# Kernel optimization log

Hardware: AMD Instinct MI355X
Metric: run time of the kernel (lower is better)

## Reference

```python
import jax, jax.numpy as jnp
import numpy as np

B, IN, H = 64, 1024, 1024

def setup_inputs() -> dict:
    key = jax.random.key(0)
    ks = jax.random.split(key, 16)
    s = 0.02
    inp = {
        'x': jax.random.normal(ks[0], (B, IN), dtype=jnp.float32),
        'C': jax.random.normal(ks[1], (B, H, H), dtype=jnp.float32) * 0.1,
        'n': jax.random.normal(ks[2], (B, H), dtype=jnp.float32) * 0.1,
        'm': jnp.zeros((B, H), dtype=jnp.float32),
    }
    names = ['i', 'f', 'o', 'q', 'k', 'v']
    for j, nm in enumerate(names):
        inp['W_' + nm] = jax.random.normal(ks[3 + 2 * j], (H, IN), dtype=jnp.float32) * s
        inp['b_' + nm] = jax.random.normal(ks[4 + 2 * j], (H,), dtype=jnp.float32) * s
    return inp

def reference(x, C, n, m, W_i, b_i, W_f, b_f, W_o, b_o, W_q, b_q, W_k, b_k, W_v, b_v):
    lin = lambda W, b: x @ W.T + b  # (B, H)
    i_tilda = lin(W_i, b_i)
    f_tilda = lin(W_f, b_f)
    o_tilda = lin(W_o, b_o)
    q_t = lin(W_q, b_q)
    k_t = lin(W_k, b_k) / jnp.sqrt(jnp.asarray(H, dtype=x.dtype))
    v_t = lin(W_v, b_v)

    f_t = jax.nn.sigmoid(f_tilda)
    o_t = jax.nn.sigmoid(o_tilda)
    # m_t = max(log(f_t) + m, log(exp(i_tilda))) = max(log_sigmoid(f_tilda) + m, i_tilda)
    m_t = jnp.maximum(jnp.log(f_t) + m, i_tilda)
    i_prime = jnp.exp(i_tilda - m_t)

    # Outer-product fast-weight update: C_t[b,i,k] = f*C + i' * v[b,i] k[b,k]
    C_t = f_t[:, :, None] * C + i_prime[:, :, None] * jnp.einsum('bi,bk->bik', v_t, k_t)
    n_t = f_t * n + i_prime * k_t

    # diagonal(n_t @ q_t.T) == per-row dot product
    normalize_inner = jnp.sum(n_t * q_t, axis=-1)
    divisor = jnp.maximum(jnp.abs(normalize_inner), jnp.ones_like(normalize_inner))
    h_tilda = jnp.einsum('bkj,bj->bk', C_t, q_t) / divisor[:, None]
    h_t = o_t * h_tilda
    return (h_t, C_t, n_t, m_t)
```

## Files before the change

### kernel.cpp

```cpp
#include <hip/hip_runtime.h>
#include <math.h>

#define BB 64
#define HH 1024
#define KK 1024

#define OFF_H ((size_t)0)
#define OFF_C ((size_t)BB * HH)
#define OFF_N (OFF_C + (size_t)BB * HH * HH)
#define OFF_M (OFF_N + (size_t)BB * HH)

#define SPLITK 4
#define GBN 32
#define GBK 64
#define NCOLBLK (6 * HH / GBN)

__device__ __forceinline__ float dot4(float4 a, float4 b) {
    return a.x * b.x + a.y * b.y + a.z * b.z + a.w * b.w;
}
__device__ __forceinline__ void fma4(float4& a, const float4 x, const float4 w) {
    a.x = fmaf(x.x, w.x, a.x);
    a.y = fmaf(x.y, w.y, a.y);
    a.z = fmaf(x.z, w.z, a.z);
    a.w = fmaf(x.w, w.w, a.w);
}

__global__ __launch_bounds__(256) void k_gemm(
    const float* __restrict__ x,
    const float* __restrict__ Wi, const float* __restrict__ Wf,
    const float* __restrict__ Wo, const float* __restrict__ Wq,
    const float* __restrict__ Wk, const float* __restrict__ Wv,
    float* __restrict__ Gp)
{
    const int cb = blockIdx.x % NCOLBLK;
    const int kc = blockIdx.x / NCOLBLK;
    const int n0 = cb * GBN;
    const int g  = n0 >> 10;
    const int h0 = n0 & (HH - 1);
    const int k0 = kc * (KK / SPLITK);

    const float* W = (g == 0) ? Wi : (g == 1) ? Wf : (g == 2) ? Wo
                   : (g == 3) ? Wq : (g == 4) ? Wk : Wv;

    const int tid = threadIdx.x;
    const int tn  = tid & 15;
    const int tm  = tid >> 4;

    __shared__ float sW[GBN][GBK + 4];

    float4 acc[4][2];
#pragma unroll
    for (int i = 0; i < 4; ++i)
#pragma unroll
        for (int j = 0; j < 2; ++j) acc[i][j] = make_float4(0.f, 0.f, 0.f, 0.f);

    for (int kk = k0; kk < k0 + KK / SPLITK; kk += GBK) {
#pragma unroll
        for (int i = 0; i < 2; ++i) {
            const int idx = tid + i * 256;
            const int c = idx >> 4;
            const int s = idx & 15;
            const float4 v = *(const float4*)(W + (size_t)(h0 + c) * KK + kk + s * 4);
            *(float4*)&sW[c][s * 4] = v;
        }
        __syncthreads();

        const float4* xr0 = (const float4*)(x + (size_t)(tm * 4 + 0) * KK + kk);
        const float4* xr1 = (const float4*)(x + (size_t)(tm * 4 + 1) * KK + kk);
        const float4* xr2 = (const float4*)(x + (size_t)(tm * 4 + 2) * KK + kk);
        const float4* xr3 = (const float4*)(x + (size_t)(tm * 4 + 3) * KK + kk);
#pragma unroll
        for (int s = 0; s < GBK / 4; ++s) {
            const float4 w0 = *(const float4*)&sW[tn * 2 + 0][s * 4];
            const float4 w1 = *(const float4*)&sW[tn * 2 + 1][s * 4];
            const float4 a0 = xr0[s];
            const float4 a1 = xr1[s];
            const float4 a2 = xr2[s];
            const float4 a3 = xr3[s];
            fma4(acc[0][0], a0, w0); fma4(acc[0][1], a0, w1);
            fma4(acc[1][0], a1, w0); fma4(acc[1][1], a1, w1);
            fma4(acc[2][0], a2, w0); fma4(acc[2][1], a2, w1);
            fma4(acc[3][0], a3, w0); fma4(acc[3][1], a3, w1);
        }
        __syncthreads();
    }

#pragma unroll
    for (int i = 0; i < 4; ++i) {
        const int b = tm * 4 + i;
        const int h = h0 + tn * 2;
        float2 v;
        v.x = acc[i][0].x + acc[i][0].y + acc[i][0].z + acc[i][0].w;
        v.y = acc[i][1].x + acc[i][1].y + acc[i][1].z + acc[i][1].w;
        *(float2*)(Gp + ((size_t)(kc * 6 + g) * BB + b) * HH + h) = v;
    }
}

__global__ __launch_bounds__(256) void k_epilogue(
    const float* __restrict__ Gp,
    const float* __restrict__ n_in, const float* __restrict__ m_in,
    const float* __restrict__ bi, const float* __restrict__ bf,
    const float* __restrict__ bo, const float* __restrict__ bq,
    const float* __restrict__ bk, const float* __restrict__ bv,
    float* __restrict__ out,
    float* __restrict__ f_s, float* __restrict__ iv_s, float* __restrict__ o_s,
    float* __restrict__ k_s, float* __restrict__ q_s, float* __restrict__ ni)
{
    const int b = blockIdx.x >> 2;
    const int h = ((blockIdx.x & 3) << 8) + threadIdx.x;
    const size_t bh = (size_t)b * HH + h;

    float gsum[6];
#pragma unroll
    for (int gg = 0; gg < 6; ++gg) {
        float s = 0.f;
#pragma unroll
        for (int kc = 0; kc < SPLITK; ++kc)
            s += Gp[((size_t)(kc * 6 + gg) * BB + b) * HH + h];
        gsum[gg] = s;
    }

    const float it = gsum[0] + bi[h];
    const float ft = gsum[1] + bf[h];
    const float ot = gsum[2] + bo[h];
    const float qt = gsum[3] + bq[h];
    const float kt = (gsum[4] + bk[h]) * 0.03125f;
    const float vt = gsum[5] + bv[h];

    const float fsig = 1.0f / (1.0f + expf(-ft));
    const float lsf  = (ft >= 0.0f) ? -log1pf(expf(-ft)) : (ft - log1pf(expf(ft)));
    const float mt   = fmaxf(lsf + m_in[bh], it);
    const float ip   = expf(it - mt);
    const float nt   = fsig * n_in[bh] + ip * kt;
    const float osg  = 1.0f / (1.0f + expf(-ot));

    out[OFF_N + bh] = nt;
    out[OFF_M + bh] = mt;
    f_s[bh]  = fsig;
    iv_s[bh] = ip * vt;
    o_s[bh]  = osg;
    k_s[bh]  = kt;
    q_s[bh]  = qt;

    float d = nt * qt;
#pragma unroll
    for (int off = 32; off >= 1; off >>= 1) d += __shfl_xor(d, off, 64);
    __shared__ float sd[4];
    if ((threadIdx.x & 63) == 0) sd[threadIdx.x >> 6] = d;
    __syncthreads();
    if (threadIdx.x == 0) atomicAdd(ni + b, sd[0] + sd[1] + sd[2] + sd[3]);
}

__global__ __launch_bounds__(256) void k2_fastweight(
    const float* __restrict__ C,
    const float* __restrict__ f_s, const float* __restrict__ iv_s,
    const float* __restrict__ o_s, const float* __restrict__ k_s,
    const float* __restrict__ q_s, const float* __restrict__ ni,
    float* __restrict__ out)
{
    const int b    = blockIdx.y;
    const int wave = threadIdx.x >> 6;
    const int lane = threadIdx.x & 63;
    const int i0   = blockIdx.x * 64 + wave * 16;

    const float4* kr = (const float4*)(k_s + (size_t)b * HH);
    const float4* qr = (const float4*)(q_s + (size_t)b * HH);
    float4 kv[4], qv[4];
#pragma unroll
    for (int s = 0; s < 4; ++s) {
        kv[s] = kr[lane + s * 64];
        qv[s] = qr[lane + s * 64];
    }
    const float inv_div = 1.0f / fmaxf(fabsf(ni[b]), 1.0f);

#pragma unroll 2
    for (int r = 0; r < 16; ++r) {
        const int row = b * HH + i0 + r;
        const float f  = f_s[row];
        const float iv = iv_s[row];
        const float4* Cr = (const float4*)(C + (size_t)row * HH);
        float4*       Ct = (float4*)(out + OFF_C + (size_t)row * HH);
        float d = 0.f;
#pragma unroll
        for (int s = 0; s < 4; ++s) {
            const float4 c4 = Cr[lane + s * 64];
            float4 o;
            o.x = fmaf(f, c4.x, iv * kv[s].x);
            o.y = fmaf(f, c4.y, iv * kv[s].y);
            o.z = fmaf(f, c4.z, iv * kv[s].z);
            o.w = fmaf(f, c4.w, iv * kv[s].w);
            Ct[lane + s * 64] = o;
            d += dot4(o, qv[s]);
        }
#pragma unroll
        for (int off = 32; off >= 1; off >>= 1) d += __shfl_xor(d, off, 64);
        if (lane == 0) out[OFF_H + row] = o_s[row] * d * inv_div;
    }
}

extern "C" void kernel_launch(void* const* d_in, const int* in_sizes, int n_in,
                              void* d_out, int out_size, void* d_ws, size_t ws_size,
                              hipStream_t stream) {
    const float* x  = (const float*)d_in[0];
    const float* C  = (const float*)d_in[1];
    const float* n  = (const float*)d_in[2];
    const float* m  = (const float*)d_in[3];
    const float* Wi = (const float*)d_in[4];  const float* bi = (const float*)d_in[5];
    const float* Wf = (const float*)d_in[6];  const float* bf = (const float*)d_in[7];
    const float* Wo = (const float*)d_in[8];  const float* bo = (const float*)d_in[9];
    const float* Wq = (const float*)d_in[10]; const float* bq = (const float*)d_in[11];
    const float* Wk = (const float*)d_in[12]; const float* bk = (const float*)d_in[13];
    const float* Wv = (const float*)d_in[14]; const float* bv = (const float*)d_in[15];

    float* out = (float*)d_out;
    float* ws  = (float*)d_ws;
    float* f_s  = ws;
    float* iv_s = ws + (size_t)BB * HH;
    float* o_s  = ws + (size_t)2 * BB * HH;
    float* k_s  = ws + (size_t)3 * BB * HH;
    float* q_s  = ws + (size_t)4 * BB * HH;
    float* ni   = ws + (size_t)5 * BB * HH;
    float* Gp   = ws + (size_t)5 * BB * HH + 256;

    hipMemsetAsync(ni, 0, BB * sizeof(float), stream);

    k_gemm<<<NCOLBLK * SPLITK, 256, 0, stream>>>(x, Wi, Wf, Wo, Wq, Wk, Wv, Gp);

    k_epilogue<<<BB * 4, 256, 0, stream>>>(Gp, n, m, bi, bf, bo, bq, bk, bv,
                                           out, f_s, iv_s, o_s, k_s, q_s, ni);

    k2_fastweight<<<dim3(16, BB), 256, 0, stream>>>(C, f_s, iv_s, o_s, k_s, q_s, ni, out);
}
```

Measured before the change: 520.2 us.

## Use nontemporal C streaming, prefetch rows, double fastweight grid, drop atomic memset

New measurement: 494.2 us. 1.05x faster.

```diff
diff --git a/kernel.cpp b/kernel.cpp
--- a/kernel.cpp
+++ b/kernel.cpp
@@ -15,6 +15,11 @@
 #define GBK 64
 #define NCOLBLK (6 * HH / GBN)
 
+typedef float __attribute__((ext_vector_type(4))) f32x4;
+
+__device__ __forceinline__ float dot4v(f32x4 a, f32x4 b) {
+    return a[0] * b[0] + a[1] * b[1] + a[2] * b[2] + a[3] * b[3];
+}
 __device__ __forceinline__ float dot4(float4 a, float4 b) {
     return a.x * b.x + a.y * b.y + a.z * b.z + a.w * b.w;
 }
@@ -23,6 +28,12 @@
     a.y = fmaf(x.y, w.y, a.y);
     a.z = fmaf(x.z, w.z, a.z);
     a.w = fmaf(x.w, w.w, a.w);
+}
+__device__ __forceinline__ f32x4 ntload4(const float* p) {
+    return __builtin_nontemporal_load((const f32x4*)p);
+}
+__device__ __forceinline__ void ntstore4(float* p, f32x4 v) {
+    __builtin_nontemporal_store(v, (f32x4*)p);
 }
 
 __global__ __launch_bounds__(256) void k_gemm(
@@ -60,8 +71,8 @@
             const int idx = tid + i * 256;
             const int c = idx >> 4;
             const int s = idx & 15;
-            const float4 v = *(const float4*)(W + (size_t)(h0 + c) * KK + kk + s * 4);
-            *(float4*)&sW[c][s * 4] = v;
+            const f32x4 v = ntload4(W + (size_t)(h0 + c) * KK + kk + s * 4);
+            *(f32x4*)&sW[c][s * 4] = v;
         }
         __syncthreads();
 
@@ -104,7 +115,7 @@
     const float* __restrict__ bk, const float* __restrict__ bv,
     float* __restrict__ out,
     float* __restrict__ f_s, float* __restrict__ iv_s, float* __restrict__ o_s,
-    float* __restrict__ k_s, float* __restrict__ q_s, float* __restrict__ ni)
+    float* __restrict__ k_s, float* __restrict__ q_s, float* __restrict__ ni4)
 {
     const int b = blockIdx.x >> 2;
     const int h = ((blockIdx.x & 3) << 8) + threadIdx.x;
@@ -148,53 +159,75 @@
     __shared__ float sd[4];
     if ((threadIdx.x & 63) == 0) sd[threadIdx.x >> 6] = d;
     __syncthreads();
-    if (threadIdx.x == 0) atomicAdd(ni + b, sd[0] + sd[1] + sd[2] + sd[3]);
+    if (threadIdx.x == 0)
+        ni4[blockIdx.x] = sd[0] + sd[1] + sd[2] + sd[3];
 }
 
 __global__ __launch_bounds__(256) void k2_fastweight(
     const float* __restrict__ C,
     const float* __restrict__ f_s, const float* __restrict__ iv_s,
     const float* __restrict__ o_s, const float* __restrict__ k_s,
-    const float* __restrict__ q_s, const float* __restrict__ ni,
+    const float* __restrict__ q_s, const float* __restrict__ ni4,
     float* __restrict__ out)
 {
     const int b    = blockIdx.y;
     const int wave = threadIdx.x >> 6;
     const int lane = threadIdx.x & 63;
-    const int i0   = blockIdx.x * 64 + wave * 16;
-
-    const float4* kr = (const float4*)(k_s + (size_t)b * HH);
-    const float4* qr = (const float4*)(q_s + (size_t)b * HH);
-    float4 kv[4], qv[4];
+    const int i0   = blockIdx.x * 32 + wave * 8;
+
+    const float* kr = k_s + (size_t)b * HH;
+    const float* qr = q_s + (size_t)b * HH;
+    f32x4 kv[4], qv[4];
 #pragma unroll
     for (int s = 0; s < 4; ++s) {
-        kv[s] = kr[lane + s * 64];
-        qv[s] = qr[lane + s * 64];
-    }
-    const float inv_div = 1.0f / fmaxf(fabsf(ni[b]), 1.0f);
-
-#pragma unroll 2
-    for (int r = 0; r < 16; ++r) {
-        const int row = b * HH + i0 + r;
-        const float f  = f_s[row];
-        const float iv = iv_s[row];
-        const float4* Cr = (const float4*)(C + (size_t)row * HH);
-        float4*       Ct = (float4*)(out + OFF_C + (size_t)row * HH);
+        kv[s] = *(const f32x4*)(kr + lane * 4 + s * 256);
+        qv[s] = *(const f32x4*)(qr + lane * 4 + s * 256);
+    }
+    const float inv_div = 1.0f /
+        fmaxf(fabsf(ni4[b * 4] + ni4[b * 4 + 1] + ni4[b * 4 + 2] + ni4[b * 4 + 3]), 1.0f);
+
+    const size_t base = (size_t)b * HH + i0;
+    float fr[8], ivr[8], ogr[8];
+#pragma unroll
+    for (int r = 0; r < 8; ++r) {
+        fr[r]  = f_s[base + r];
+        ivr[r] = iv_s[base + r];
+        ogr[r] = o_s[base + r] * inv_div;
+    }
+
+    const float* Crow = C + base * HH;
+    float* Ctrow = out + OFF_C + base * HH;
+
+    f32x4 c_cur[4], c_nxt[4];
+#pragma unroll
+    for (int s = 0; s < 4; ++s) c_cur[s] = ntload4(Crow + lane * 4 + s * 256);
+
+#pragma unroll
+    for (int r = 0; r < 8; ++r) {
+        if (r < 7) {
+            const float* Cn = Crow + (size_t)(r + 1) * HH;
+#pragma unroll
+            for (int s = 0; s < 4; ++s) c_nxt[s] = ntload4(Cn + lane * 4 + s * 256);
+        }
+        const float f  = fr[r];
+        const float iv = ivr[r];
+        float* Ct = Ctrow + (size_t)r * HH;
         float d = 0.f;
 #pragma unroll
         for (int s = 0; s < 4; ++s) {
-            const float4 c4 = Cr[lane + s * 64];
-            float4 o;
-            o.x = fmaf(f, c4.x, iv * kv[s].x);
-            o.y = fmaf(f, c4.y, iv * kv[s].y);
-            o.z = fmaf(f, c4.z, iv * kv[s].z);
-            o.w = fmaf(f, c4.w, iv * kv[s].w);
-            Ct[lane + s * 64] = o;
-            d += dot4(o, qv[s]);
+            f32x4 o;
+            o[0] = fmaf(f, c_cur[s][0], iv * kv[s][0]);
+            o[1] = fmaf(f, c_cur[s][1], iv * kv[s][1]);
+            o[2] = fmaf(f, c_cur[s][2], iv * kv[s][2]);
+            o[3] = fmaf(f, c_cur[s][3], iv * kv[s][3]);
+            ntstore4(Ct + lane * 4 + s * 256, o);
+            d += dot4v(o, qv[s]);
         }
 #pragma unroll
         for (int off = 32; off >= 1; off >>= 1) d += __shfl_xor(d, off, 64);
-        if (lane == 0) out[OFF_H + row] = o_s[row] * d * inv_div;
+        if (lane == 0) out[OFF_H + base + r] = ogr[r] * d;
+#pragma unroll
+        for (int s = 0; s < 4; ++s) c_cur[s] = c_nxt[s];
     }
 }
 
@@ -219,15 +252,13 @@
     float* o_s  = ws + (size_t)2 * BB * HH;
     float* k_s  = ws + (size_t)3 * BB * HH;
     float* q_s  = ws + (size_t)4 * BB * HH;
-    float* ni   = ws + (size_t)5 * BB * HH;
+    float* ni4  = ws + (size_t)5 * BB * HH;
     float* Gp   = ws + (size_t)5 * BB * HH + 256;
 
-    hipMemsetAsync(ni, 0, BB * sizeof(float), stream);
-
     k_gemm<<<NCOLBLK * SPLITK, 256, 0, stream>>>(x, Wi, Wf, Wo, Wq, Wk, Wv, Gp);
 
     k_epilogue<<<BB * 4, 256, 0, stream>>>(Gp, n, m, bi, bf, bo, bq, bk, bv,
-                                           out, f_s, iv_s, o_s, k_s, q_s, ni);
-
-    k2_fastweight<<<dim3(16, BB), 256, 0, stream>>>(C, f_s, iv_s, o_s, k_s, q_s, ni, out);
-}
+                                           out, f_s, iv_s, o_s, k_s, q_s, ni4);
+
+    k2_fastweight<<<dim3(32, BB), 256, 0, stream>>>(C, f_s, iv_s, o_s, k_s, q_s, ni4, out);
+}
```
